# Optimization experiments

Hardware: AMD Instinct MI355X
Metric: run time of the kernel (lower is better)

The kernel has to match this reference:

```python
import jax, jax.numpy as jnp
import numpy as np

IN_F = 4096
OUT_F = 11008
BATCH = 4
SEQ = 2048


def setup_inputs() -> dict:
    key = jax.random.key(0)
    kx, kw, ks = jax.random.split(key, 3)
    x = jax.random.normal(kx, (BATCH, SEQ, IN_F), dtype=jnp.float32)
    # simulated int4 weights stored in an int container, range [0, 16)
    W_q = jax.random.randint(kw, (OUT_F, IN_F), 0, 16, dtype=jnp.int32)
    scale = jax.random.uniform(ks, (OUT_F,), dtype=jnp.float32)
    return {"x": x, "W_q": W_q, "scale": scale}


def reference(x, W_q, scale):
    # dequantize: per-output-channel scale, then y = x @ W_fp^T
    W_fp = W_q.astype(jnp.float32) * scale[:, None]  # [out, in]
    return jnp.einsum('bsi,oi->bso', x, W_fp)
```

## Files before the change

### kernel.cpp

```cpp
#include <hip/hip_runtime.h>
#include <math.h>

#define M_DIM 8192
#define N_DIM 11008
#define K_DIM 4096

#define BM 256
#define BN 128
#define BKB 64
#define NT (K_DIM / BKB)
#define NBN (N_DIM / BN)
#define NWG ((M_DIM / BM) * NBN)

#define CHUNK_A_STRIDE (M_DIM * 16)
#define CHUNK_B_STRIDE (N_DIM * 16)

typedef int int4v __attribute__((ext_vector_type(4)));
typedef int int16v __attribute__((ext_vector_type(16)));

__device__ __forceinline__ void async_copy16(const void* g, void* l) {
  __builtin_amdgcn_global_load_lds(
      (const __attribute__((address_space(1))) void*)g,
      (__attribute__((address_space(3))) void*)l, 16, 0, 0);
}

__global__ __launch_bounds__(256) void quant_x(const float* __restrict__ x,
                                               signed char* __restrict__ xqt,
                                               float* __restrict__ sx) {
  __shared__ float wred[4];
  const int row = blockIdx.x;
  const int tid = threadIdx.x;
  const float4* src = (const float4*)(x + (size_t)row * K_DIM) + tid * 4;
  float4 v0 = src[0], v1 = src[1], v2 = src[2], v3 = src[3];

  float m = 0.f;
#define MX4(V) m = fmaxf(m, fmaxf(fmaxf(fabsf(V.x), fabsf(V.y)), fmaxf(fabsf(V.z), fabsf(V.w))))
  MX4(v0); MX4(v1); MX4(v2); MX4(v3);
#undef MX4
#pragma unroll
  for (int off = 32; off >= 1; off >>= 1)
    m = fmaxf(m, __shfl_xor(m, off, 64));
  if ((tid & 63) == 0) wred[tid >> 6] = m;
  __syncthreads();
  float smax = fmaxf(fmaxf(wred[0], wred[1]), fmaxf(wred[2], wred[3]));
  smax = fmaxf(smax, 1e-20f);
  const float inv = 127.f / smax;

  int4v o;
#define Q4(V, G) o[G] = ((int)rintf(V.x * inv) & 255) | (((int)rintf(V.y * inv) & 255) << 8) | \
                        (((int)rintf(V.z * inv) & 255) << 16) | (((int)rintf(V.w * inv) & 255) << 24)
  Q4(v0, 0); Q4(v1, 1); Q4(v2, 2); Q4(v3, 3);
#undef Q4
  ((int4v*)xqt)[(size_t)tid * M_DIM + row] = o;
  if (tid == 0) sx[row] = smax / 127.f;
}

__global__ __launch_bounds__(256) void pack_w(const int* __restrict__ in,
                                              signed char* __restrict__ wqt) {
  const int cg = blockIdx.x % (N_DIM / 256);
  const int c = blockIdx.x / (N_DIM / 256);
  const int col = cg * 256 + threadIdx.x;
  const int4* src = (const int4*)(in + (size_t)col * K_DIM + c * 16);
  int4 a = src[0], b = src[1], d = src[2], e = src[3];
  int4v o;
  o[0] = a.x | (a.y << 8) | (a.z << 16) | (a.w << 24);
  o[1] = b.x | (b.y << 8) | (b.z << 16) | (b.w << 24);
  o[2] = d.x | (d.y << 8) | (d.z << 16) | (d.w << 24);
  o[3] = e.x | (e.y << 8) | (e.z << 16) | (e.w << 24);
  ((int4v*)wqt)[(size_t)c * N_DIM + col] = o;
}

__global__ __launch_bounds__(512, 4) void gemm_i8(
    const signed char* __restrict__ A, const signed char* __restrict__ B,
    const float* __restrict__ scale, const float* __restrict__ sx,
    float* __restrict__ out) {
  __shared__ __align__(16) char smw[16384];
  const int tid = threadIdx.x;
  const int lane = tid & 63;
  const int wv = tid >> 6;
  const int wr = wv >> 1, wc = wv & 1;
  const int l31 = lane & 31;
  const int h = lane >> 5;

  int id = blockIdx.x;
  id = (id & 7) * (NWG / 8) + (id >> 3);
  const int bn = (id % NBN) * BN;
  const int bm = (id / NBN) * BM;

  int16v acc[2][2] = {};

  const signed char* Abase =
      A + (size_t)h * CHUNK_A_STRIDE + (size_t)(bm + wr * 64 + l31) * 16;
  const signed char* Bsrc0 =
      B + (size_t)(tid >> 7) * CHUNK_B_STRIDE + (size_t)(bn + (tid & 127)) * 16;

#define STAGE_B(T, OFF) \
  async_copy16(Bsrc0 + (size_t)(4 * (T)) * CHUNK_B_STRIDE, smw + (OFF) + tid * 16)

#define LOAD_A(T, SET)                                                        \
  _Pragma("unroll") for (int ks = 0; ks < 2; ++ks)                            \
  _Pragma("unroll") for (int mi = 0; mi < 2; ++mi)                            \
    SET[ks][mi] = *(const int4v*)(Abase +                                     \
        (size_t)(4 * (T) + 2 * ks) * CHUNK_A_STRIDE + mi * 32 * 16);

#define COMPUTE(SET, OFF)                                                     \
  _Pragma("unroll") for (int ks = 0; ks < 2; ++ks) {                          \
    int4v bfr[2];                                                             \
    _Pragma("unroll") for (int ni = 0; ni < 2; ++ni)                          \
      bfr[ni] = *(const int4v*)(smw + (OFF) + (2 * ks + h) * 2048 +           \
                                (wc * 64 + ni * 32 + l31) * 16);              \
    __builtin_amdgcn_s_setprio(1);                                            \
    _Pragma("unroll") for (int mi = 0; mi < 2; ++mi)                          \
    _Pragma("unroll") for (int ni = 0; ni < 2; ++ni)                          \
      acc[mi][ni] = __builtin_amdgcn_mfma_i32_32x32x32_i8(                    \
          SET[ks][mi], bfr[ni], acc[mi][ni], 0, 0, 0);                        \
    __builtin_amdgcn_s_setprio(0);                                            \
  }

  int4v AX[2][2], AY[2][2];

  STAGE_B(0, 0);
  LOAD_A(0, AX);
  asm volatile("s_waitcnt vmcnt(0)" ::: "memory");
  __builtin_amdgcn_s_barrier();

#pragma unroll 1
  for (int t = 0; t < NT; t += 2) {
    STAGE_B(t + 1, 8192);
    LOAD_A(t + 1, AY);
    COMPUTE(AX, 0);
    asm volatile("s_waitcnt vmcnt(0)" ::: "memory");
    __builtin_amdgcn_s_barrier();

    if (t + 2 < NT) {
      STAGE_B(t + 2, 0);
      LOAD_A(t + 2, AX);
    }
    COMPUTE(AY, 8192);
    if (t + 2 < NT) {
      asm volatile("s_waitcnt vmcnt(0)" ::: "memory");
      __builtin_amdgcn_s_barrier();
    }
  }

  const int ocol0 = bn + wc * 64 + l31;
  const int orow0 = bm + wr * 64 + 4 * h;
#pragma unroll
  for (int ni = 0; ni < 2; ++ni) {
    const float sc = scale[ocol0 + ni * 32];
#pragma unroll
    for (int mi = 0; mi < 2; ++mi) {
#pragma unroll
      for (int reg = 0; reg < 16; ++reg) {
        const int row = orow0 + mi * 32 + (reg & 3) + 8 * (reg >> 2);
        out[(size_t)row * N_DIM + ocol0 + ni * 32] =
            (float)acc[mi][ni][reg] * sx[row] * sc;
      }
    }
  }
#undef STAGE_B
#undef LOAD_A
#undef COMPUTE
}

__global__ __launch_bounds__(256) void gemm_fallback(
    const float* __restrict__ X, const int* __restrict__ Wq,
    const float* __restrict__ scale, float* __restrict__ out) {
  __shared__ float Xs[64][17];
  __shared__ float Ws[64][17];
  const int tid = threadIdx.x;
  const int tn = blockIdx.x % (N_DIM / 64);
  const int tm = blockIdx.x / (N_DIM / 64);
  const int tr = tid >> 4, tc = tid & 15;
  float acc[4][4] = {};
  for (int k0 = 0; k0 < K_DIM; k0 += 16) {
#pragma unroll
    for (int i = 0; i < 4; ++i) {
      int idx = tid + i * 256;
      int r = idx >> 4, c = idx & 15;
      Xs[r][c] = X[(size_t)(tm * 64 + r) * K_DIM + k0 + c];
      Ws[r][c] = (float)Wq[(size_t)(tn * 64 + r) * K_DIM + k0 + c];
    }
    __syncthreads();
#pragma unroll
    for (int kk = 0; kk < 16; ++kk)
#pragma unroll
      for (int i = 0; i < 4; ++i) {
        float a = Xs[tr * 4 + i][kk];
#pragma unroll
        for (int j = 0; j < 4; ++j) acc[i][j] += a * Ws[tc * 4 + j][kk];
      }
    __syncthreads();
  }
#pragma unroll
  for (int i = 0; i < 4; ++i)
#pragma unroll
    for (int j = 0; j < 4; ++j) {
      int row = tm * 64 + tr * 4 + i, col = tn * 64 + tc * 4 + j;
      out[(size_t)row * N_DIM + col] = acc[i][j] * scale[col];
    }
}

extern "C" void kernel_launch(void* const* d_in, const int* in_sizes, int n_in,
                              void* d_out, int out_size, void* d_ws, size_t ws_size,
                              hipStream_t stream) {
  const float* x = (const float*)d_in[0];
  const int* Wq = (const int*)d_in[1];
  const float* scale = (const float*)d_in[2];
  float* out = (float*)d_out;

  const size_t XN = (size_t)M_DIM * K_DIM;
  const size_t WN = (size_t)N_DIM * K_DIM;
  const size_t need = XN + WN + M_DIM * sizeof(float);

  if (ws_size >= need) {
    signed char* xqt = (signed char*)d_ws;
    signed char* wqt = xqt + XN;
    float* sx = (float*)(wqt + WN);
    quant_x<<<M_DIM, 256, 0, stream>>>(x, xqt, sx);
    pack_w<<<(N_DIM / 256) * 256, 256, 0, stream>>>(Wq, wqt);
    gemm_i8<<<NWG, 512, 0, stream>>>(xqt, wqt, scale, sx, out);
  } else {
    gemm_fallback<<<(N_DIM / 64) * (M_DIM / 64), 256, 0, stream>>>(x, Wq, scale, out);
  }
}
```

Measured before the change: 513.1 us.

## Deepen B-tile LDS pipeline to four buffers with partial vmcnt waits

Expands shared memory to four 8 KB B buffers and prefetches B two tiles ahead, replacing full vmcnt(0) drains with partial waits so later loads stay in flight across the barrier. The goal is to hide global-load latency better in the int8 MFMA GEMM main loop. It doubles LDS per workgroup, which may cut occupancy under the 4-blocks-per-CU launch bound. The waitcnt counts must exactly match the outstanding load accounting to stay correct.

```diff
diff --git a/kernel.cpp b/kernel.cpp
--- a/kernel.cpp
+++ b/kernel.cpp
@@ -74,7 +74,7 @@
     const signed char* __restrict__ A, const signed char* __restrict__ B,
     const float* __restrict__ scale, const float* __restrict__ sx,
     float* __restrict__ out) {
-  __shared__ __align__(16) char smw[16384];
+  __shared__ __align__(16) char smw[32768];
   const int tid = threadIdx.x;
   const int lane = tid & 63;
   const int wv = tid >> 6;
@@ -94,8 +94,9 @@
   const signed char* Bsrc0 =
       B + (size_t)(tid >> 7) * CHUNK_B_STRIDE + (size_t)(bn + (tid & 127)) * 16;
 
-#define STAGE_B(T, OFF) \
-  async_copy16(Bsrc0 + (size_t)(4 * (T)) * CHUNK_B_STRIDE, smw + (OFF) + tid * 16)
+#define STAGE_B(T) \
+  async_copy16(Bsrc0 + (size_t)(4 * (T)) * CHUNK_B_STRIDE, \
+               smw + (((T) & 3) * 8192) + tid * 16)
 
 #define LOAD_A(T, SET)                                                        \
   _Pragma("unroll") for (int ks = 0; ks < 2; ++ks)                            \
@@ -103,11 +104,11 @@
     SET[ks][mi] = *(const int4v*)(Abase +                                     \
         (size_t)(4 * (T) + 2 * ks) * CHUNK_A_STRIDE + mi * 32 * 16);
 
-#define COMPUTE(SET, OFF)                                                     \
+#define COMPUTE(SET, BOFF)                                                    \
   _Pragma("unroll") for (int ks = 0; ks < 2; ++ks) {                          \
     int4v bfr[2];                                                             \
     _Pragma("unroll") for (int ni = 0; ni < 2; ++ni)                          \
-      bfr[ni] = *(const int4v*)(smw + (OFF) + (2 * ks + h) * 2048 +           \
+      bfr[ni] = *(const int4v*)(smw + (BOFF) + (2 * ks + h) * 2048 +          \
                                 (wc * 64 + ni * 32 + l31) * 16);              \
     __builtin_amdgcn_s_setprio(1);                                            \
     _Pragma("unroll") for (int mi = 0; mi < 2; ++mi)                          \
@@ -117,30 +118,34 @@
     __builtin_amdgcn_s_setprio(0);                                            \
   }
 
+#define TILE_BODY(T, CURA, NEXTA)                                             \
+  {                                                                           \
+    if ((T) + 2 < NT) STAGE_B((T) + 2);                                       \
+    __builtin_amdgcn_sched_barrier(0);     \
+    if ((T) + 1 < NT) LOAD_A((T) + 1, NEXTA);                                 \
+    COMPUTE(CURA, ((T) & 3) * 8192);                                          \
+    if ((T) + 1 < NT) {                                                       \
+      if ((T) + 2 < NT)                                                       \
+        asm volatile("s_waitcnt vmcnt(5)" ::: "memory");                      \
+      else                                                                    \
+        asm volatile("s_waitcnt vmcnt(4)" ::: "memory");                      \
+      __builtin_amdgcn_s_barrier();                                           \
+    }                                                                         \
+  }
+
   int4v AX[2][2], AY[2][2];
 
-  STAGE_B(0, 0);
+  STAGE_B(0);
+  STAGE_B(1);
+  __builtin_amdgcn_sched_barrier(0);
   LOAD_A(0, AX);
-  asm volatile("s_waitcnt vmcnt(0)" ::: "memory");
+  asm volatile("s_waitcnt vmcnt(5)" ::: "memory");
   __builtin_amdgcn_s_barrier();
 
 #pragma unroll 1
   for (int t = 0; t < NT; t += 2) {
-    STAGE_B(t + 1, 8192);
-    LOAD_A(t + 1, AY);
-    COMPUTE(AX, 0);
-    asm volatile("s_waitcnt vmcnt(0)" ::: "memory");
-    __builtin_amdgcn_s_barrier();
-
-    if (t + 2 < NT) {
-      STAGE_B(t + 2, 0);
-      LOAD_A(t + 2, AX);
-    }
-    COMPUTE(AY, 8192);
-    if (t + 2 < NT) {
-      asm volatile("s_waitcnt vmcnt(0)" ::: "memory");
-      __builtin_amdgcn_s_barrier();
-    }
+    TILE_BODY(t, AX, AY);
+    TILE_BODY(t + 1, AY, AX);
   }
 
   const int ocol0 = bn + wc * 64 + l31;
@@ -161,6 +166,7 @@
 #undef STAGE_B
 #undef LOAD_A
 #undef COMPUTE
+#undef TILE_BODY
 }
 
 __global__ __launch_bounds__(256) void gemm_fallback(
```

Result: no change. 516.2 us (+0.6%).
